# Kernel tuning notes

Measured on AMD Instinct MI355X. Metric: run time of the kernel, lower is better.

The kernel has to match this reference:

```python
import jax, jax.numpy as jnp
import numpy as np

B, S, N, HID = 4, 512, 128, 64


def setup_inputs() -> dict:
    key = jax.random.key(0)
    ks = jax.random.split(key, 32)
    def rn(k, shape, scale=0.1):
        return jax.random.normal(k, shape, dtype=jnp.float32) * scale
    adj = jax.random.randint(ks[0], (N, N), 0, 2).astype(jnp.int32)
    adj = adj.at[jnp.arange(N), jnp.arange(N)].set(1)  # self loops
    inp = {
        'x': jax.random.normal(ks[1], (B, S, N, 1), dtype=jnp.float32),
        'adj': adj,
        'emb_w': rn(ks[2], (1, 16)), 'emb_b': jnp.zeros((16,), jnp.float32),
        'gat1_W': rn(ks[3], (16, 16)), 'gat1_a': rn(ks[4], (32, 1)),
        'gat2_W': rn(ks[5], (16, 8)), 'gat2_a': rn(ks[6], (16, 1)),
        'Wih0': rn(ks[7], (4 * HID, N)), 'Whh0': rn(ks[8], (4 * HID, HID)),
        'bih0': jnp.zeros((4 * HID,), jnp.float32), 'bhh0': jnp.zeros((4 * HID,), jnp.float32),
        'Wih1': rn(ks[9], (4 * HID, HID)), 'Whh1': rn(ks[10], (4 * HID, HID)),
        'bih1': jnp.zeros((4 * HID,), jnp.float32), 'bhh1': jnp.zeros((4 * HID,), jnp.float32),
    }
    comb = HID + 8 * N
    for i, name in enumerate(['dir', 'ret', 'vol']):
        o = 2 if name == 'vol' else 1
        inp[name + '_w1'] = rn(ks[11 + 4 * i], (comb, 32))
        inp[name + '_b1'] = jnp.zeros((32,), jnp.float32)
        inp[name + '_w2'] = rn(ks[12 + 4 * i], (32, o))
        inp[name + '_b2'] = jnp.zeros((o,), jnp.float32)
    return inp


def _gat(h, W, a, mask):
    # e_ij = leakyrelu(a1 . Wh_i + a2 . Wh_j): avoid torch's [M,N,N,2F] concat.
    Wh = h @ W                                  # [M, N, F]
    Fo = W.shape[1]
    f1 = Wh @ a[:Fo]                            # [M, N, 1]
    f2 = Wh @ a[Fo:]                            # [M, N, 1]
    e = jax.nn.leaky_relu(f1 + jnp.swapaxes(f2, 1, 2), 0.2)  # [M, N, N]
    e = jnp.where(mask, e, jnp.float32(-9e15))
    attn = jax.nn.softmax(e, axis=2)
    return attn @ Wh                            # [M, N, F]


def _lstm_layer(xs, Wih, Whh, bih, bhh):
    # xs: [S, B, I]; PyTorch gate order i, f, g, o
    Bsz = xs.shape[1]
    Hd = Whh.shape[1]
    def step(carry, xt):
        h, c = carry
        g = xt @ Wih.T + h @ Whh.T + bih + bhh
        i, f, gg, o = jnp.split(g, 4, axis=-1)
        c = jax.nn.sigmoid(f) * c + jax.nn.sigmoid(i) * jnp.tanh(gg)
        h = jax.nn.sigmoid(o) * jnp.tanh(c)
        return (h, c), h
    init = (jnp.zeros((Bsz, Hd), xs.dtype), jnp.zeros((Bsz, Hd), xs.dtype))
    _, hs = jax.lax.scan(step, init, xs)
    return hs


def reference(x, adj, emb_w, emb_b, gat1_W, gat1_a, gat2_W, gat2_a,
              Wih0, Whh0, bih0, bhh0, Wih1, Whh1, bih1, bhh1,
              dir_w1, dir_b1, dir_w2, dir_b2,
              ret_w1, ret_b1, ret_w2, ret_b2,
              vol_w1, vol_b1, vol_w2, vol_b2):
    Bz, Sz, Nz, _ = x.shape
    mask = (adj > 0)[None]                      # [1, N, N], broadcast over B*S
    xe = (x @ emb_w + emb_b).reshape(Bz * Sz, Nz, 16)
    xg = jax.nn.elu(_gat(xe, gat1_W, gat1_a, mask))   # gat1 concat=True -> elu
    xg = _gat(xg, gat2_W, gat2_a, mask)               # gat2 concat=False
    xg_out = xg.reshape(Bz, Sz, Nz * 8)[:, -1, :]
    xs = jnp.swapaxes(x.reshape(Bz, Sz, Nz), 0, 1)    # [S, B, N]
    hs = _lstm_layer(xs, Wih0, Whh0, bih0, bhh0)
    hs = _lstm_layer(hs, Wih1, Whh1, bih1, bhh1)      # inter-layer dropout off (eval)
    xl_out = hs[-1]                                   # [B, 64]
    c = jnp.concatenate([xl_out, xg_out], axis=1)     # [B, 64 + 8N]
    def head(w1, b1, w2, b2):
        return jax.nn.relu(c @ w1 + b1) @ w2 + b2
    return (head(dir_w1, dir_b1, dir_w2, dir_b2),
            head(ret_w1, ret_b1, ret_w2, ret_b2),
            head(vol_w1, vol_b1, vol_w2, vol_b2))
```

## Files before the change

kernel.cpp:

```cpp
#include <hip/hip_runtime.h>

#define SEQ   512
#define BATCH 4
#define NN    128
#define HID   64
#define G4    256
#define MAGIC 0x13579BDF

typedef _Float16 half2v __attribute__((ext_vector_type(2)));

__device__ __forceinline__ float frcp(float x)  { return __builtin_amdgcn_rcpf(x); }
__device__ __forceinline__ float fsigm(float x) { return frcp(1.f + __expf(-x)); }
__device__ __forceinline__ float ftanh(float x) { return 1.f - 2.f * frcp(1.f + __expf(2.f * x)); }
__device__ __forceinline__ float lrelu(float x) { return x > 0.f ? x : 0.2f * x; }
__device__ __forceinline__ float dot4f(float4 w, float4 h) {
  return fmaf(w.x, h.x, fmaf(w.y, h.y, fmaf(w.z, h.z, w.w * h.w)));
}
__device__ __forceinline__ void pin4(float4& v) {
  asm volatile("" : "+v"(v.x), "+v"(v.y), "+v"(v.z), "+v"(v.w));
}
__device__ __forceinline__ float qsum(float x) {
  x += __int_as_float(__builtin_amdgcn_update_dpp(
      0, __float_as_int(x), 0xB1, 0xF, 0xF, true));
  x += __int_as_float(__builtin_amdgcn_update_dpp(
      0, __float_as_int(x), 0x4E, 0xF, 0xF, true));
  return x;
}
__device__ __forceinline__ half2v u2h(unsigned u) {
  return __builtin_bit_cast(half2v, u);
}
__device__ __forceinline__ half2v pk16(float lo, float hi) {
  return __builtin_bit_cast(half2v, __builtin_amdgcn_cvt_pkrtz(lo, hi));
}
__device__ __forceinline__ float fdot2(half2v a, half2v b, float c) {
#if __has_builtin(__builtin_amdgcn_fdot2)
  return __builtin_amdgcn_fdot2(a, b, c, false);
#else
  float d = c;
  asm("v_dot2_f32_f16 %0, %1, %2, %0" : "+v"(d) : "v"(a), "v"(b));
  return d;
#endif
}
__device__ __forceinline__ float dot8h(const half2v* w, const uint4& a,
                                       const uint4& b, float acc) {
  acc = fdot2(w[0], u2h(a.x), acc);
  acc = fdot2(w[1], u2h(a.y), acc);
  acc = fdot2(w[2], u2h(a.z), acc);
  acc = fdot2(w[3], u2h(a.w), acc);
  acc = fdot2(w[4], u2h(b.x), acc);
  acc = fdot2(w[5], u2h(b.y), acc);
  acc = fdot2(w[6], u2h(b.z), acc);
  acc = fdot2(w[7], u2h(b.w), acc);
  return acc;
}

#define BAR_LDS() asm volatile("s_waitcnt lgkmcnt(0)\n\ts_barrier" ::: "memory")

__global__ __attribute__((amdgpu_flat_work_group_size(768, 768),
                          amdgpu_waves_per_eu(3, 3)))
void fused_all(
    const float* __restrict__ x, const int* __restrict__ adj,
    const float* __restrict__ emb_w, const float* __restrict__ emb_b,
    const float* __restrict__ W1, const float* __restrict__ a1,
    const float* __restrict__ W2, const float* __restrict__ a2,
    const float* __restrict__ Wih0, const float* __restrict__ Whh0,
    const float* __restrict__ bih0, const float* __restrict__ bhh0,
    const float* __restrict__ Wih1, const float* __restrict__ Whh1,
    const float* __restrict__ bih1, const float* __restrict__ bhh1,
    const float* __restrict__ dw1, const float* __restrict__ db1,
    const float* __restrict__ dw2, const float* __restrict__ db2,
    const float* __restrict__ rw1, const float* __restrict__ rb1,
    const float* __restrict__ rw2, const float* __restrict__ rb2,
    const float* __restrict__ vw1, const float* __restrict__ vb1,
    const float* __restrict__ vw2, const float* __restrict__ vb2,
    float* __restrict__ X0T, float* __restrict__ xg,
    int* __restrict__ flags, float* __restrict__ out)
{
  const int bid = blockIdx.x;
  const int tid = threadIdx.x;

  if (bid >= 4) {
    const int c = bid - 4;
    __shared__ __align__(16) float xls[NN];
    {
      const int g = tid >> 1, half = tid & 1;
      float4 w4[16];
      if (tid < 512) {
        const float4* wp = reinterpret_cast<const float4*>(Wih0 + g * NN + half * 64);
#pragma unroll
        for (int i = 0; i < 16; ++i) w4[i] = wp[i];
#pragma unroll
        for (int i = 0; i < 16; ++i) pin4(w4[i]);
      }
      const float bsum = (tid < 512) ? (bih0[g] + bhh0[g]) : 0.f;
      for (int phase = 0; phase < 4; ++phase) {
        const int T = c + 128 * phase;
        for (int bb = 0; bb < BATCH; ++bb) {
          if (tid < NN) xls[tid] = x[(bb * SEQ + T) * NN + tid];
          __syncthreads();
          if (tid < 512) {
            const float4* hp = reinterpret_cast<const float4*>(&xls[half * 64]);
            float p0 = 0.f, p1 = 0.f, p2 = 0.f, p3 = 0.f;
#pragma unroll
            for (int k = 0; k < 16; k += 4) {
              p0 += dot4f(w4[k],     hp[k]);
              p1 += dot4f(w4[k + 1], hp[k + 1]);
              p2 += dot4f(w4[k + 2], hp[k + 2]);
              p3 += dot4f(w4[k + 3], hp[k + 3]);
            }
            float p = (p0 + p1) + (p2 + p3);
            p += __shfl_xor(p, 1);
            if (half == 0)
              X0T[(4 * T + bb) * G4 + (g & 63) * 4 + (g >> 6)] = p + bsum;
          }
          __syncthreads();
        }
        if (tid == 0 && phase == 0)
          __hip_atomic_store(&flags[c], MAGIC, __ATOMIC_RELEASE,
                             __HIP_MEMORY_SCOPE_AGENT);
        if (tid == 0 && phase == 3)
          __hip_atomic_store(&flags[128 + c], MAGIC, __ATOMIC_RELEASE,
                             __HIP_MEMORY_SCOPE_AGENT);
      }
    }
    if (bid >= 8) return;

    const int b = bid - 4;
    __shared__ float adjm[NN * 129];
    __shared__ __align__(16) float gxls[NN];
    __shared__ float u[16], v[16];
    __shared__ float Wh2[NN][9];
    __shared__ float f1b[NN], f2b[NN];
    __shared__ float p[NN];

    for (int idx = tid; idx < NN * NN; idx += 768)
      adjm[(idx >> 7) * 129 + (idx & 127)] = (adj[idx] > 0) ? 1.f : 0.f;
    if (tid < NN) gxls[tid] = x[(b * SEQ + (SEQ - 1)) * NN + tid];
    if (tid < 16) {
      float uu = 0.f, vv = 0.f;
      for (int fp = 0; fp < 16; ++fp) {
        uu += emb_w[fp] * W1[fp * 16 + tid];
        vv += emb_b[fp] * W1[fp * 16 + tid];
      }
      u[tid] = uu; v[tid] = vv;
    }
    __syncthreads();
    float s1 = 0.f, t1 = 0.f, s2 = 0.f, t2 = 0.f;
    for (int f = 0; f < 16; ++f) {
      s1 += u[f] * a1[f];      t1 += v[f] * a1[f];
      s2 += u[f] * a1[16 + f]; t2 += v[f] * a1[16 + f];
    }
    if (tid < NN) {
      const int i = tid;
      const float f1i = gxls[i] * s1 + t1;
      float m = -1e30f;
      for (int j = 0; j < NN; ++j)
        if (adjm[i * 129 + j] != 0.f)
          m = fmaxf(m, lrelu(f1i + gxls[j] * s2 + t2));
      float ssum = 0.f, ps = 0.f;
      for (int j = 0; j < NN; ++j)
        if (adjm[i * 129 + j] != 0.f) {
          const float wgt = __expf(lrelu(f1i + gxls[j] * s2 + t2) - m);
          ssum += wgt; ps += wgt * gxls[j];
        }
      p[i] = ps / ssum;
    }
    __syncthreads();
    if (tid < NN) {
      const int i = tid;
      float xg1[16];
#pragma unroll
      for (int f = 0; f < 16; ++f) {
        const float ov = p[i] * u[f] + v[f];
        xg1[f] = ov > 0.f ? ov : expm1f(ov);
      }
      float wrow[8];
#pragma unroll
      for (int f2 = 0; f2 < 8; ++f2) wrow[f2] = 0.f;
#pragma unroll
      for (int f = 0; f < 16; ++f) {
        const float xv = xg1[f];
#pragma unroll
        for (int f2 = 0; f2 < 8; ++f2) wrow[f2] += xv * W2[f * 8 + f2];
      }
      float fb1 = 0.f, fb2 = 0.f;
#pragma unroll
      for (int f2 = 0; f2 < 8; ++f2) {
        Wh2[i][f2] = wrow[f2];
        fb1 += wrow[f2] * a2[f2];
        fb2 += wrow[f2] * a2[8 + f2];
      }
      f1b[i] = fb1; f2b[i] = fb2;
    }
    __syncthreads();
    if (tid < NN) {
      const int i = tid;
      const float fi = f1b[i];
      float m = -1e30f;
      for (int j = 0; j < NN; ++j)
        if (adjm[i * 129 + j] != 0.f)
          m = fmaxf(m, lrelu(fi + f2b[j]));
      float ssum = 0.f;
      float o[8];
#pragma unroll
      for (int f2 = 0; f2 < 8; ++f2) o[f2] = 0.f;
      for (int j = 0; j < NN; ++j)
        if (adjm[i * 129 + j] != 0.f) {
          const float wgt = __expf(lrelu(fi + f2b[j]) - m);
          ssum += wgt;
#pragma unroll
          for (int f2 = 0; f2 < 8; ++f2) o[f2] += wgt * Wh2[j][f2];
        }
      const float inv = 1.f / ssum;
#pragma unroll
      for (int f2 = 0; f2 < 8; ++f2)
        xg[b * (NN * 8) + i * 8 + f2] = o[f2] * inv;
    }
    __syncthreads();
    if (tid == 0)
      __hip_atomic_store(&flags[256 + b], MAGIC, __ATOMIC_RELEASE,
                         __HIP_MEMORY_SCOPE_AGENT);
    return;
  }

  const int b   = bid;
  const int t   = tid;
  const int grp = t >> 8;
  const int r   = t & 255;
  const int uu  = r >> 2, q2 = r & 3;

  __shared__ __align__(16) half2v hb16[2][2][HID / 2];
  __shared__ __align__(16) float P1[2][G4];
  __shared__ float cbuf[1088];
  __shared__ float hidc[96];

  const float* Wsrc = (grp == 0) ? Whh0 : (grp == 1) ? Wih1 : Whh1;
  half2v w16[4][8];
#pragma unroll
  for (int j = 0; j < 4; ++j) {
    const float* wr = Wsrc + (uu + 64 * j) * HID + 16 * q2;
#pragma unroll
    for (int c = 0; c < 4; ++c) {
      const float4 wv = *reinterpret_cast<const float4*>(wr + 4 * c);
      w16[j][2 * c]     = half2v{(_Float16)wv.x, (_Float16)wv.y};
      w16[j][2 * c + 1] = half2v{(_Float16)wv.z, (_Float16)wv.w};
    }
  }
  float4 b1v = make_float4(0.f, 0.f, 0.f, 0.f);
  if (grp == 2) {
    b1v.x = bih1[uu]       + bhh1[uu];
    b1v.y = bih1[uu + 64]  + bhh1[uu + 64];
    b1v.z = bih1[uu + 128] + bhh1[uu + 128];
    b1v.w = bih1[uu + 192] + bhh1[uu + 192];
  }

  if (t < 128) reinterpret_cast<unsigned*>(hb16)[t] = 0u;
  float cst = 0.f;
  const float* X0b = X0T + b * G4 + uu * 4;

  int c_ok;
  {
    if (t < 32) {
      while (__hip_atomic_fetch_add(&flags[t], 0, __ATOMIC_ACQUIRE,
                                    __HIP_MEMORY_SCOPE_AGENT) != MAGIC) {}
    }
    __syncthreads();
    c_ok = 31;
  }

  const int lay = (grp == 2) ? 1 : 0;
  const uint4* hpA = reinterpret_cast<const uint4*>(&hb16[0][lay][0]) + 2 * q2;
  const uint4* hpB = reinterpret_cast<const uint4*>(&hb16[1][lay][0]) + 2 * q2;

  float4 xa0 = make_float4(0.f, 0.f, 0.f, 0.f), xa1 = xa0, xa2 = xa0, xa3 = xa0;
  if (grp == 0) {
    xa0 = *reinterpret_cast<const float4*>(X0b + 0 * (BATCH * G4));
    xa1 = *reinterpret_cast<const float4*>(X0b + 1 * (BATCH * G4));
    xa2 = *reinterpret_cast<const float4*>(X0b + 2 * (BATCH * G4));
    xa3 = *reinterpret_cast<const float4*>(X0b + 3 * (BATCH * G4));
  }

#define PACK_WRITE(LAYER, WB, HV)                                              \
  do {                                                                         \
    const float pr_ = __int_as_float(__builtin_amdgcn_update_dpp(              \
        0, __float_as_int(HV), 0x141, 0xF, 0xF, true));                        \
    if ((r & 7) == 0)                                                          \
      hb16[WB][LAYER][r >> 3] = pk16((HV), pr_);                               \
  } while (0)

#define LSTM_STEP(TT, RB, WB, XV)                                              \
  do {                                                                         \
    const uint4* hp = (RB) ? hpB : hpA;                                        \
    const uint4 ua = hp[0];                                                    \
    const uint4 ub = hp[1];                                                    \
    float4 p1v = make_float4(0.f, 0.f, 0.f, 0.f);                              \
    if (grp == 2) p1v = *reinterpret_cast<const float4*>(&P1[1 - (RB)][uu * 4]); \
    const float A0 = dot8h(w16[0], ua, ub, 0.f);                               \
    const float A1 = dot8h(w16[1], ua, ub, 0.f);                               \
    const float A2 = dot8h(w16[2], ua, ub, 0.f);                               \
    const float A3 = dot8h(w16[3], ua, ub, 0.f);                               \
    const float S0 = qsum(A0), S1 = qsum(A1), S2 = qsum(A2), S3 = qsum(A3);    \
    if (grp == 0) {                                                            \
      if ((TT) < SEQ) {                                                        \
        const float gi = fsigm(S0 + (XV).x);                                   \
        const float gf = fsigm(S1 + (XV).y);                                   \
        const float gg = ftanh(S2 + (XV).z);                                   \
        const float go = fsigm(S3 + (XV).w);                                   \
        cst = fmaf(gf, cst, gi * gg);                                          \
        const float hv = go * ftanh(cst);                                      \
        PACK_WRITE(0, WB, hv);                                                 \
      }                                                                        \
    } else if (grp == 1) {                                                     \
      if ((TT) >= 1 && (TT) <= SEQ) {                                          \
        const float sel = (q2 == 0) ? S0 : (q2 == 1) ? S1 : (q2 == 2) ? S2 : S3; \
        P1[RB][r] = sel;                                                       \
      }                                                                        \
    } else {                                                                   \
      if ((TT) >= 2) {                                                         \
        const float gi = fsigm(S0 + p1v.x + b1v.x);                            \
        const float gf = fsigm(S1 + p1v.y + b1v.y);                            \
        const float gg = ftanh(S2 + p1v.z + b1v.z);                            \
        const float go = fsigm(S3 + p1v.w + b1v.w);                            \
        cst = fmaf(gf, cst, gi * gg);                                          \
        const float hv = go * ftanh(cst);                                      \
        PACK_WRITE(1, WB, hv);                                                 \
      }                                                                        \
    }                                                                          \
    BAR_LDS();                                                                 \
  } while (0)

  for (int tt = 0; tt < SEQ; tt += 4) {
    if (tt + 36 > c_ok && c_ok < 255) {
      const int base = c_ok + 1;
      if (t < 32 && base + t <= 255) {
        while (__hip_atomic_fetch_add(&flags[base + t], 0, __ATOMIC_ACQUIRE,
                                      __HIP_MEMORY_SCOPE_AGENT) != MAGIC) {}
      }
      __syncthreads();
      c_ok = (base + 31 < 255) ? base + 31 : 255;
    }
#pragma unroll
    for (int j = 0; j < 4; ++j) {
      asm volatile("" : "+v"(w16[j][0]), "+v"(w16[j][1]), "+v"(w16[j][2]),
                        "+v"(w16[j][3]), "+v"(w16[j][4]), "+v"(w16[j][5]),
                        "+v"(w16[j][6]), "+v"(w16[j][7]));
    }
    float4 xb0 = xa0, xb1 = xa1, xb2 = xa2, xb3 = xa3;
    if (grp == 0 && tt + 4 < SEQ) {
      xb0 = *reinterpret_cast<const float4*>(X0b + (tt + 4) * (BATCH * G4));
      xb1 = *reinterpret_cast<const float4*>(X0b + (tt + 5) * (BATCH * G4));
      xb2 = *reinterpret_cast<const float4*>(X0b + (tt + 6) * (BATCH * G4));
      xb3 = *reinterpret_cast<const float4*>(X0b + (tt + 7) * (BATCH * G4));
    }
    LSTM_STEP(tt + 0, 0, 1, xa0);
    LSTM_STEP(tt + 1, 1, 0, xa1);
    LSTM_STEP(tt + 2, 0, 1, xa2);
    LSTM_STEP(tt + 3, 1, 0, xa3);
    xa0 = xb0; xa1 = xb1; xa2 = xb2; xa3 = xb3;
  }
  LSTM_STEP(512, 0, 1, xa0);
  LSTM_STEP(513, 1, 0, xa1);
#undef LSTM_STEP
#undef PACK_WRITE

  if (t == 0) {
    while (__hip_atomic_fetch_add(&flags[256 + b], 0, __ATOMIC_ACQUIRE,
                                  __HIP_MEMORY_SCOPE_AGENT) != MAGIC) {}
  }
  __syncthreads();

  if (t < 64) {
    const _Float16* hh = reinterpret_cast<const _Float16*>(&hb16[0][1][0]);
    cbuf[t] = (float)hh[t];
  }
  for (int k = t; k < 1024; k += 768) cbuf[64 + k] = xg[b * 1024 + k];
  __syncthreads();
  if (t < 96) {
    const int head = t >> 5, h = t & 31;
    const float* w1 = (head == 0) ? dw1 : (head == 1) ? rw1 : vw1;
    const float* b1 = (head == 0) ? db1 : (head == 1) ? rb1 : vb1;
    float a0 = 0.f, a1v = 0.f, a2v = 0.f, a3v = 0.f;
    for (int k = 0; k < 1088; k += 4) {
      a0  = fmaf(cbuf[k],     w1[k * 32 + h],       a0);
      a1v = fmaf(cbuf[k + 1], w1[(k + 1) * 32 + h], a1v);
      a2v = fmaf(cbuf[k + 2], w1[(k + 2) * 32 + h], a2v);
      a3v = fmaf(cbuf[k + 3], w1[(k + 3) * 32 + h], a3v);
    }
    hidc[head * 32 + h] = fmaxf(b1[h] + ((a0 + a1v) + (a2v + a3v)), 0.f);
  }
  __syncthreads();
  if (t < 4) {
    const int head2 = (t < 2) ? t : 2;
    const int o = (t < 2) ? 0 : (t - 2);
    const int odim = (t < 2) ? 1 : 2;
    const float* w2  = (head2 == 0) ? dw2 : (head2 == 1) ? rw2 : vw2;
    const float* b2p = (head2 == 0) ? db2 : (head2 == 1) ? rb2 : vb2;
    float acc = b2p[o];
    for (int hh = 0; hh < 32; ++hh)
      acc = fmaf(hidc[head2 * 32 + hh], w2[hh * odim + o], acc);
    const int off = (t == 0) ? b : (t == 1) ? (4 + b) : (8 + 2 * b + o);
    out[off] = acc;
  }
}

extern "C" void kernel_launch(void* const* d_in, const int* in_sizes, int n_in,
                              void* d_out, int out_size, void* d_ws, size_t ws_size,
                              hipStream_t stream) {
  const float* x     = (const float*)d_in[0];
  const int*   adj   = (const int*)  d_in[1];
  const float* emb_w = (const float*)d_in[2];
  const float* emb_b = (const float*)d_in[3];
  const float* g1W   = (const float*)d_in[4];
  const float* g1a   = (const float*)d_in[5];
  const float* g2W   = (const float*)d_in[6];
  const float* g2a   = (const float*)d_in[7];
  const float* Wih0  = (const float*)d_in[8];
  const float* Whh0  = (const float*)d_in[9];
  const float* bih0  = (const float*)d_in[10];
  const float* bhh0  = (const float*)d_in[11];
  const float* Wih1  = (const float*)d_in[12];
  const float* Whh1  = (const float*)d_in[13];
  const float* bih1  = (const float*)d_in[14];
  const float* bhh1  = (const float*)d_in[15];
  const float* dw1 = (const float*)d_in[16]; const float* db1 = (const float*)d_in[17];
  const float* dw2 = (const float*)d_in[18]; const float* db2 = (const float*)d_in[19];
  const float* rw1 = (const float*)d_in[20]; const float* rb1 = (const float*)d_in[21];
  const float* rw2 = (const float*)d_in[22]; const float* rb2 = (const float*)d_in[23];
  const float* vw1 = (const float*)d_in[24]; const float* vb1 = (const float*)d_in[25];
  const float* vw2 = (const float*)d_in[26]; const float* vb2 = (const float*)d_in[27];

  float* ws = (float*)d_ws;
  float* X0 = ws;
  float* xg = ws + SEQ * BATCH * G4;
  int*  flg = (int*)(xg + BATCH * NN * 8);
  float* out = (float*)d_out;

  hipLaunchKernelGGL(fused_all, dim3(132), dim3(768), 0, stream,
                     x, adj, emb_w, emb_b, g1W, g1a, g2W, g2a,
                     Wih0, Whh0, bih0, bhh0, Wih1, Whh1, bih1, bhh1,
                     dw1, db1, dw2, db2, rw1, rb1, rw2, rb2,
                     vw1, vb1, vw2, vb2,
                     X0, xg, flg, out);
}
```

Measured before the change: 445.4 us.

## Collapse three LSTM wave-groups into one 256-thread block per batch

The workgroup drops from 768 to 256 threads. Each LSTM thread now holds all three recurrent weight sets (Whh0, Wih1, Whh1) in registers and computes both layers itself, which removes the P1 shared-memory handoff and the one-step pipeline skew between groups. The Wih0 precompute blocks use one thread per gate row with a full 128-wide dot product instead of splitting rows across thread pairs. This cuts barrier participants and cross-group LDS traffic, at the cost of three times the weight registers and per-thread work on the serial critical path.

```diff
diff --git a/kernel.cpp b/kernel.cpp
--- a/kernel.cpp
+++ b/kernel.cpp
@@ -56,8 +56,8 @@
 
 #define BAR_LDS() asm volatile("s_waitcnt lgkmcnt(0)\n\ts_barrier" ::: "memory")
 
-__global__ __attribute__((amdgpu_flat_work_group_size(768, 768),
-                          amdgpu_waves_per_eu(3, 3)))
+__global__ __attribute__((amdgpu_flat_work_group_size(256, 256),
+                          amdgpu_waves_per_eu(1, 4)))
 void fused_all(
     const float* __restrict__ x, const int* __restrict__ adj,
     const float* __restrict__ emb_w, const float* __restrict__ emb_b,
@@ -83,35 +83,33 @@
     const int c = bid - 4;
     __shared__ __align__(16) float xls[NN];
     {
-      const int g = tid >> 1, half = tid & 1;
-      float4 w4[16];
-      if (tid < 512) {
-        const float4* wp = reinterpret_cast<const float4*>(Wih0 + g * NN + half * 64);
-#pragma unroll
-        for (int i = 0; i < 16; ++i) w4[i] = wp[i];
-#pragma unroll
-        for (int i = 0; i < 16; ++i) pin4(w4[i]);
-      }
-      const float bsum = (tid < 512) ? (bih0[g] + bhh0[g]) : 0.f;
+      const int g = tid;
+      float4 w4[32];
+      {
+        const float4* wp = reinterpret_cast<const float4*>(Wih0 + g * NN);
+#pragma unroll
+        for (int i = 0; i < 32; ++i) w4[i] = wp[i];
+#pragma unroll
+        for (int i = 0; i < 32; ++i) pin4(w4[i]);
+      }
+      const float bsum = bih0[g] + bhh0[g];
       for (int phase = 0; phase < 4; ++phase) {
         const int T = c + 128 * phase;
         for (int bb = 0; bb < BATCH; ++bb) {
           if (tid < NN) xls[tid] = x[(bb * SEQ + T) * NN + tid];
           __syncthreads();
-          if (tid < 512) {
-            const float4* hp = reinterpret_cast<const float4*>(&xls[half * 64]);
+          {
+            const float4* hp = reinterpret_cast<const float4*>(xls);
             float p0 = 0.f, p1 = 0.f, p2 = 0.f, p3 = 0.f;
 #pragma unroll
-            for (int k = 0; k < 16; k += 4) {
+            for (int k = 0; k < 32; k += 4) {
               p0 += dot4f(w4[k],     hp[k]);
               p1 += dot4f(w4[k + 1], hp[k + 1]);
               p2 += dot4f(w4[k + 2], hp[k + 2]);
               p3 += dot4f(w4[k + 3], hp[k + 3]);
             }
-            float p = (p0 + p1) + (p2 + p3);
-            p += __shfl_xor(p, 1);
-            if (half == 0)
-              X0T[(4 * T + bb) * G4 + (g & 63) * 4 + (g >> 6)] = p + bsum;
+            X0T[(4 * T + bb) * G4 + (g & 63) * 4 + (g >> 6)] =
+                ((p0 + p1) + (p2 + p3)) + bsum;
           }
           __syncthreads();
         }
@@ -133,7 +131,7 @@
     __shared__ float f1b[NN], f2b[NN];
     __shared__ float p[NN];
 
-    for (int idx = tid; idx < NN * NN; idx += 768)
+    for (int idx = tid; idx < NN * NN; idx += 256)
       adjm[(idx >> 7) * 129 + (idx & 127)] = (adj[idx] > 0) ? 1.f : 0.f;
     if (tid < NN) gxls[tid] = x[(b * SEQ + (SEQ - 1)) * NN + tid];
     if (tid < 16) {
@@ -225,37 +223,41 @@
 
   const int b   = bid;
   const int t   = tid;
-  const int grp = t >> 8;
-  const int r   = t & 255;
-  const int uu  = r >> 2, q2 = r & 3;
+  const int uu  = t >> 2, q2 = t & 3;
+  const int r   = t;
 
   __shared__ __align__(16) half2v hb16[2][2][HID / 2];
-  __shared__ __align__(16) float P1[2][G4];
   __shared__ float cbuf[1088];
   __shared__ float hidc[96];
 
-  const float* Wsrc = (grp == 0) ? Whh0 : (grp == 1) ? Wih1 : Whh1;
-  half2v w16[4][8];
+  half2v wA[4][8], wB[4][8], wC[4][8];
 #pragma unroll
   for (int j = 0; j < 4; ++j) {
-    const float* wr = Wsrc + (uu + 64 * j) * HID + 16 * q2;
+    const int row = (uu + 64 * j) * HID + 16 * q2;
+    const float* wa = Whh0 + row;
+    const float* wb = Wih1 + row;
+    const float* wc = Whh1 + row;
 #pragma unroll
     for (int c = 0; c < 4; ++c) {
-      const float4 wv = *reinterpret_cast<const float4*>(wr + 4 * c);
-      w16[j][2 * c]     = half2v{(_Float16)wv.x, (_Float16)wv.y};
-      w16[j][2 * c + 1] = half2v{(_Float16)wv.z, (_Float16)wv.w};
-    }
-  }
-  float4 b1v = make_float4(0.f, 0.f, 0.f, 0.f);
-  if (grp == 2) {
-    b1v.x = bih1[uu]       + bhh1[uu];
-    b1v.y = bih1[uu + 64]  + bhh1[uu + 64];
-    b1v.z = bih1[uu + 128] + bhh1[uu + 128];
-    b1v.w = bih1[uu + 192] + bhh1[uu + 192];
-  }
+      const float4 va = *reinterpret_cast<const float4*>(wa + 4 * c);
+      const float4 vb = *reinterpret_cast<const float4*>(wb + 4 * c);
+      const float4 vc = *reinterpret_cast<const float4*>(wc + 4 * c);
+      wA[j][2 * c]     = half2v{(_Float16)va.x, (_Float16)va.y};
+      wA[j][2 * c + 1] = half2v{(_Float16)va.z, (_Float16)va.w};
+      wB[j][2 * c]     = half2v{(_Float16)vb.x, (_Float16)vb.y};
+      wB[j][2 * c + 1] = half2v{(_Float16)vb.z, (_Float16)vb.w};
+      wC[j][2 * c]     = half2v{(_Float16)vc.x, (_Float16)vc.y};
+      wC[j][2 * c + 1] = half2v{(_Float16)vc.z, (_Float16)vc.w};
+    }
+  }
+  float4 b1v;
+  b1v.x = bih1[uu]       + bhh1[uu];
+  b1v.y = bih1[uu + 64]  + bhh1[uu + 64];
+  b1v.z = bih1[uu + 128] + bhh1[uu + 128];
+  b1v.w = bih1[uu + 192] + bhh1[uu + 192];
 
   if (t < 128) reinterpret_cast<unsigned*>(hb16)[t] = 0u;
-  float cst = 0.f;
+  float cst0 = 0.f, cst1 = 0.f;
   const float* X0b = X0T + b * G4 + uu * 4;
 
   int c_ok;
@@ -268,17 +270,15 @@
     c_ok = 31;
   }
 
-  const int lay = (grp == 2) ? 1 : 0;
-  const uint4* hpA = reinterpret_cast<const uint4*>(&hb16[0][lay][0]) + 2 * q2;
-  const uint4* hpB = reinterpret_cast<const uint4*>(&hb16[1][lay][0]) + 2 * q2;
-
-  float4 xa0 = make_float4(0.f, 0.f, 0.f, 0.f), xa1 = xa0, xa2 = xa0, xa3 = xa0;
-  if (grp == 0) {
-    xa0 = *reinterpret_cast<const float4*>(X0b + 0 * (BATCH * G4));
-    xa1 = *reinterpret_cast<const float4*>(X0b + 1 * (BATCH * G4));
-    xa2 = *reinterpret_cast<const float4*>(X0b + 2 * (BATCH * G4));
-    xa3 = *reinterpret_cast<const float4*>(X0b + 3 * (BATCH * G4));
-  }
+  const uint4* h0A = reinterpret_cast<const uint4*>(&hb16[0][0][0]) + 2 * q2;
+  const uint4* h0B = reinterpret_cast<const uint4*>(&hb16[1][0][0]) + 2 * q2;
+  const uint4* h1A = reinterpret_cast<const uint4*>(&hb16[0][1][0]) + 2 * q2;
+  const uint4* h1B = reinterpret_cast<const uint4*>(&hb16[1][1][0]) + 2 * q2;
+
+  float4 xa0 = *reinterpret_cast<const float4*>(X0b + 0 * (BATCH * G4));
+  float4 xa1 = *reinterpret_cast<const float4*>(X0b + 1 * (BATCH * G4));
+  float4 xa2 = *reinterpret_cast<const float4*>(X0b + 2 * (BATCH * G4));
+  float4 xa3 = *reinterpret_cast<const float4*>(X0b + 3 * (BATCH * G4));
 
 #define PACK_WRITE(LAYER, WB, HV)                                              \
   do {                                                                         \
@@ -290,41 +290,42 @@
 
 #define LSTM_STEP(TT, RB, WB, XV)                                              \
   do {                                                                         \
-    const uint4* hp = (RB) ? hpB : hpA;                                        \
-    const uint4 ua = hp[0];                                                    \
-    const uint4 ub = hp[1];                                                    \
-    float4 p1v = make_float4(0.f, 0.f, 0.f, 0.f);                              \
-    if (grp == 2) p1v = *reinterpret_cast<const float4*>(&P1[1 - (RB)][uu * 4]); \
-    const float A0 = dot8h(w16[0], ua, ub, 0.f);                               \
-    const float A1 = dot8h(w16[1], ua, ub, 0.f);                               \
-    const float A2 = dot8h(w16[2], ua, ub, 0.f);                               \
-    const float A3 = dot8h(w16[3], ua, ub, 0.f);                               \
-    const float S0 = qsum(A0), S1 = qsum(A1), S2 = qsum(A2), S3 = qsum(A3);    \
-    if (grp == 0) {                                                            \
-      if ((TT) < SEQ) {                                                        \
-        const float gi = fsigm(S0 + (XV).x);                                   \
-        const float gf = fsigm(S1 + (XV).y);                                   \
-        const float gg = ftanh(S2 + (XV).z);                                   \
-        const float go = fsigm(S3 + (XV).w);                                   \
-        cst = fmaf(gf, cst, gi * gg);                                          \
-        const float hv = go * ftanh(cst);                                      \
-        PACK_WRITE(0, WB, hv);                                                 \
-      }                                                                        \
-    } else if (grp == 1) {                                                     \
-      if ((TT) >= 1 && (TT) <= SEQ) {                                          \
-        const float sel = (q2 == 0) ? S0 : (q2 == 1) ? S1 : (q2 == 2) ? S2 : S3; \
-        P1[RB][r] = sel;                                                       \
-      }                                                                        \
-    } else {                                                                   \
-      if ((TT) >= 2) {                                                         \
-        const float gi = fsigm(S0 + p1v.x + b1v.x);                            \
-        const float gf = fsigm(S1 + p1v.y + b1v.y);                            \
-        const float gg = ftanh(S2 + p1v.z + b1v.z);                            \
-        const float go = fsigm(S3 + p1v.w + b1v.w);                            \
-        cst = fmaf(gf, cst, gi * gg);                                          \
-        const float hv = go * ftanh(cst);                                      \
-        PACK_WRITE(1, WB, hv);                                                 \
-      }                                                                        \
+    const uint4* h0p = (RB) ? h0B : h0A;                                       \
+    const uint4* h1p = (RB) ? h1B : h1A;                                       \
+    const uint4 ha = h0p[0], hbb = h0p[1];                                     \
+    const uint4 ga = h1p[0], gbb = h1p[1];                                     \
+    float A0 = dot8h(wA[0], ha, hbb, 0.f);                                     \
+    float A1 = dot8h(wA[1], ha, hbb, 0.f);                                     \
+    float A2 = dot8h(wA[2], ha, hbb, 0.f);                                     \
+    float A3 = dot8h(wA[3], ha, hbb, 0.f);                                     \
+    float B0 = dot8h(wB[0], ha, hbb, 0.f);                                     \
+    float B1 = dot8h(wB[1], ha, hbb, 0.f);                                     \
+    float B2 = dot8h(wB[2], ha, hbb, 0.f);                                     \
+    float B3 = dot8h(wB[3], ha, hbb, 0.f);                                     \
+    float C0 = dot8h(wC[0], ga, gbb, 0.f);                                     \
+    float C1 = dot8h(wC[1], ga, gbb, 0.f);                                     \
+    float C2 = dot8h(wC[2], ga, gbb, 0.f);                                     \
+    float C3 = dot8h(wC[3], ga, gbb, 0.f);                                     \
+    const float SA0 = qsum(A0), SA1 = qsum(A1), SA2 = qsum(A2), SA3 = qsum(A3);\
+    if ((TT) < SEQ) {                                                          \
+      const float gi = fsigm(SA0 + (XV).x);                                    \
+      const float gf = fsigm(SA1 + (XV).y);                                    \
+      const float gg = ftanh(SA2 + (XV).z);                                    \
+      const float go = fsigm(SA3 + (XV).w);                                    \
+      cst0 = fmaf(gf, cst0, gi * gg);                                          \
+      const float hv = go * ftanh(cst0);                                       \
+      PACK_WRITE(0, WB, hv);                                                   \
+    }                                                                          \
+    const float SB0 = qsum(B0), SB1 = qsum(B1), SB2 = qsum(B2), SB3 = qsum(B3);\
+    const float SC0 = qsum(C0), SC1 = qsum(C1), SC2 = qsum(C2), SC3 = qsum(C3);\
+    if ((TT) >= 1) {                                                           \
+      const float gi = fsigm(SC0 + SB0 + b1v.x);                               \
+      const float gf = fsigm(SC1 + SB1 + b1v.y);                               \
+      const float gg = ftanh(SC2 + SB2 + b1v.z);                               \
+      const float go = fsigm(SC3 + SB3 + b1v.w);                               \
+      cst1 = fmaf(gf, cst1, gi * gg);                                          \
+      const float hv = go * ftanh(cst1);                                       \
+      PACK_WRITE(1, WB, hv);                                                   \
     }                                                                          \
     BAR_LDS();                                                                 \
   } while (0)
@@ -341,12 +342,18 @@
     }
 #pragma unroll
     for (int j = 0; j < 4; ++j) {
-      asm volatile("" : "+v"(w16[j][0]), "+v"(w16[j][1]), "+v"(w16[j][2]),
-                        "+v"(w16[j][3]), "+v"(w16[j][4]), "+v"(w16[j][5]),
-                        "+v"(w16[j][6]), "+v"(w16[j][7]));
+      asm volatile("" : "+v"(wA[j][0]), "+v"(wA[j][1]), "+v"(wA[j][2]),
+                        "+v"(wA[j][3]), "+v"(wA[j][4]), "+v"(wA[j][5]),
+                        "+v"(wA[j][6]), "+v"(wA[j][7]));
+      asm volatile("" : "+v"(wB[j][0]), "+v"(wB[j][1]), "+v"(wB[j][2]),
+                        "+v"(wB[j][3]), "+v"(wB[j][4]), "+v"(wB[j][5]),
+                        "+v"(wB[j][6]), "+v"(wB[j][7]));
+      asm volatile("" : "+v"(wC[j][0]), "+v"(wC[j][1]), "+v"(wC[j][2]),
+                        "+v"(wC[j][3]), "+v"(wC[j][4]), "+v"(wC[j][5]),
+                        "+v"(wC[j][6]), "+v"(wC[j][7]));
     }
     float4 xb0 = xa0, xb1 = xa1, xb2 = xa2, xb3 = xa3;
-    if (grp == 0 && tt + 4 < SEQ) {
+    if (tt + 4 < SEQ) {
       xb0 = *reinterpret_cast<const float4*>(X0b + (tt + 4) * (BATCH * G4));
       xb1 = *reinterpret_cast<const float4*>(X0b + (tt + 5) * (BATCH * G4));
       xb2 = *reinterpret_cast<const float4*>(X0b + (tt + 6) * (BATCH * G4));
@@ -359,7 +366,6 @@
     xa0 = xb0; xa1 = xb1; xa2 = xb2; xa3 = xb3;
   }
   LSTM_STEP(512, 0, 1, xa0);
-  LSTM_STEP(513, 1, 0, xa1);
 #undef LSTM_STEP
 #undef PACK_WRITE
 
@@ -370,10 +376,10 @@
   __syncthreads();
 
   if (t < 64) {
-    const _Float16* hh = reinterpret_cast<const _Float16*>(&hb16[0][1][0]);
+    const _Float16* hh = reinterpret_cast<const _Float16*>(&hb16[1][1][0]);
     cbuf[t] = (float)hh[t];
   }
-  for (int k = t; k < 1024; k += 768) cbuf[64 + k] = xg[b * 1024 + k];
+  for (int k = t; k < 1024; k += 256) cbuf[64 + k] = xg[b * 1024 + k];
   __syncthreads();
   if (t < 96) {
     const int head = t >> 5, h = t & 31;
@@ -435,7 +441,7 @@
   int*  flg = (int*)(xg + BATCH * NN * 8);
   float* out = (float*)d_out;
 
-  hipLaunchKernelGGL(fused_all, dim3(132), dim3(768), 0, stream,
+  hipLaunchKernelGGL(fused_all, dim3(132), dim3(256), 0, stream,
                      x, adj, emb_w, emb_b, g1W, g1a, g2W, g2a,
                      Wih0, Whh0, bih0, bhh0, Wih1, Whh1, bih1, bhh1,
                      dw1, db1, dw2, db2, rw1, rb1, rw2, rb2,
```

Result: faster. 412.8 us (-7.3%).
